# Kernel tuning notes

Measured on AMD Instinct MI355X. Metric: run time of the kernel, lower is better.

The kernel has to match this reference:

```python
import jax, jax.numpy as jnp
import numpy as np

N_NODES = 100000
IN_F = 512
HID = 256
HEADS = 1
CLASSES = 40
ALPHA = 0.5
EPS = 1e-5


def layer_norm(x, g, b):
    mu = jnp.mean(x, axis=-1, keepdims=True)
    var = jnp.mean(jnp.square(x - mu), axis=-1, keepdims=True)
    return g * (x - mu) / jnp.sqrt(var + EPS) + b


def full_attention_conv(qs, ks, vs):
    # qs, ks, vs: [N, H, D]; global (Frobenius) L2 normalization as in torch.norm(p=2)
    qs = qs / jnp.linalg.norm(qs.reshape(-1))
    ks = ks / jnp.linalg.norm(ks.reshape(-1))
    N = qs.shape[0]
    kvs = jnp.einsum('lhm,lhd->hmd', ks, vs)                  # [H, D, D]
    attention_num = jnp.einsum('nhm,hmd->nhd', qs, kvs) + N * vs
    ks_sum = jnp.sum(ks, axis=0)                              # [H, D]
    attention_normalizer = jnp.einsum('nhm,hm->nh', qs, ks_sum)[..., None] + N
    return attention_num / attention_normalizer               # [N, H, D]


def trans_layer(h, prev, Wq, bq, Wk, bk, Wv, bv, ln_g, ln_b):
    N = h.shape[0]
    q = (h @ Wq + bq).reshape(N, HEADS, HID)
    k = (h @ Wk + bk).reshape(N, HEADS, HID)
    v = (h @ Wv + bv).reshape(N, HEADS, HID)
    attn = full_attention_conv(q, k, v).mean(axis=1)          # [N, HID]
    h = ALPHA * attn + (1.0 - ALPHA) * prev
    return layer_norm(h, ln_g, ln_b)


def setup_inputs() -> dict:
    key = jax.random.key(0)
    ks = jax.random.split(key, 16)
    s_in = 1.0 / np.sqrt(IN_F)
    s_h = 1.0 / np.sqrt(HID)
    d = {
        'x': jax.random.normal(ks[0], (N_NODES, IN_F), jnp.float32),
        'edge_index': jax.random.randint(ks[1], (2, 1600000), 0, N_NODES, jnp.int64),
        'W_in': jax.random.normal(ks[2], (IN_F, HID), jnp.float32) * s_in,
        'b_in': jnp.zeros((HID,), jnp.float32),
        'ln0_g': jnp.ones((HID,), jnp.float32),
        'ln0_b': jnp.zeros((HID,), jnp.float32),
        'Wq0': jax.random.normal(ks[3], (HID, HID * HEADS), jnp.float32) * s_h,
        'bq0': jnp.zeros((HID * HEADS,), jnp.float32),
        'Wk0': jax.random.normal(ks[4], (HID, HID * HEADS), jnp.float32) * s_h,
        'bk0': jnp.zeros((HID * HEADS,), jnp.float32),
        'Wv0': jax.random.normal(ks[5], (HID, HID * HEADS), jnp.float32) * s_h,
        'bv0': jnp.zeros((HID * HEADS,), jnp.float32),
        'ln1_g': jnp.ones((HID,), jnp.float32),
        'ln1_b': jnp.zeros((HID,), jnp.float32),
        'Wq1': jax.random.normal(ks[6], (HID, HID * HEADS), jnp.float32) * s_h,
        'bq1': jnp.zeros((HID * HEADS,), jnp.float32),
        'Wk1': jax.random.normal(ks[7], (HID, HID * HEADS), jnp.float32) * s_h,
        'bk1': jnp.zeros((HID * HEADS,), jnp.float32),
        'Wv1': jax.random.normal(ks[8], (HID, HID * HEADS), jnp.float32) * s_h,
        'bv1': jnp.zeros((HID * HEADS,), jnp.float32),
        'ln2_g': jnp.ones((HID,), jnp.float32),
        'ln2_b': jnp.zeros((HID,), jnp.float32),
        'W_out': jax.random.normal(ks[9], (HID, CLASSES), jnp.float32) * s_h,
        'b_out': jnp.zeros((CLASSES,), jnp.float32),
    }
    return d


def reference(x, edge_index, W_in, b_in, ln0_g, ln0_b,
              Wq0, bq0, Wk0, bk0, Wv0, bv0, ln1_g, ln1_b,
              Wq1, bq1, Wk1, bk1, Wv1, bv1, ln2_g, ln2_b,
              W_out, b_out):
    # SGFormer forward with use_graph=False, eval mode (dropout no-op).
    h = jax.nn.relu(layer_norm(x @ W_in + b_in, ln0_g, ln0_b))
    prev = h
    h = trans_layer(h, prev, Wq0, bq0, Wk0, bk0, Wv0, bv0, ln1_g, ln1_b)
    prev = h
    h = trans_layer(h, prev, Wq1, bq1, Wk1, bk1, Wv1, bv1, ln2_g, ln2_b)
    return h @ W_out + b_out  # [N, CLASSES]
```

## Files before the change

kernel.cpp:

```cpp
#include <hip/hip_runtime.h>


typedef __attribute__((ext_vector_type(8))) short short8;
typedef __attribute__((ext_vector_type(4))) short short4v;
typedef __attribute__((ext_vector_type(4))) float floatx4;

__device__ __forceinline__ float bf2f(short u) {
    union { unsigned int i; float f; } v;
    v.i = ((unsigned int)(unsigned short)u) << 16;
    return v.f;
}
__device__ __forceinline__ short f2bf(float f) {
    union { float f; unsigned int i; } v; v.f = f;
    unsigned int b = v.i + 0x7fffu + ((v.i >> 16) & 1u);
    return (short)(b >> 16);
}

#define HID 256
#define MROWS 100000
#define GBLK 1563
#define EPSLN 1e-5f

__device__ __forceinline__ size_t fragoff(int blk, int w, int m, int n, int lane) {
    return (((((size_t)blk * 4 + w) * 4 + m) * 4 + n) * 64 + lane);
}

__device__ __forceinline__ void stage_a256(const short* __restrict__ A, short* As,
                                           int row0, int wave, int lane)
{
    const int base = wave * 512;
#pragma unroll
    for (int it = 0; it < 8; ++it) {
        int J = base + it * 64 + lane;
        int row = J >> 5, jj = J & 31;
        int c = jj ^ (row & 31);
        int rowg = min(row0 + row, MROWS - 1);
        const short* gp = A + (size_t)rowg * HID + c * 8;
        __builtin_amdgcn_global_load_lds(
            (const __attribute__((address_space(1))) void*)gp,
            (__attribute__((address_space(3))) void*)&As[(size_t)(base + it * 64) * 8],
            16, 0, 0);
    }
}
__device__ __forceinline__ void stage_lin256(const short* __restrict__ A, short* As,
                                             int row0, int wave, int lane)
{
    const int base = wave * 512;
#pragma unroll
    for (int it = 0; it < 8; ++it) {
        int J = base + it * 64 + lane;
        int row = J >> 5, jj = J & 31;
        int rowg = min(row0 + row, MROWS - 1);
        const short* gp = A + (size_t)rowg * HID + jj * 8;
        __builtin_amdgcn_global_load_lds(
            (const __attribute__((address_space(1))) void*)gp,
            (__attribute__((address_space(3))) void*)&As[(size_t)(base + it * 64) * 8],
            16, 0, 0);
    }
}
__device__ __forceinline__ short8 read_a256(const short* As, int m, int ki, int quad, int l15)
{
    int row = m * 16 + l15;
    int phys = (ki * 4 + quad) ^ (row & 31);
    return *(const short8*)&As[((size_t)row * 32 + phys) * 8];
}

__global__ __launch_bounds__(256, 3)
void qkv_kernel(const short* __restrict__ h,
                const short* __restrict__ BTq, const short* __restrict__ BTk,
                const short* __restrict__ BTv,
                const float* __restrict__ bq, const float* __restrict__ bk,
                const float* __restrict__ bv,
                short* __restrict__ qO, short* __restrict__ kF, short* __restrict__ vF,
                float* __restrict__ sqq, float* __restrict__ sqk,
                float* __restrict__ ksum)
{
    __shared__ short As[64 * 256];
    __shared__ short Cb[16 * 264];

    const int tid = threadIdx.x, wave = tid >> 6, lane = tid & 63;
    const int quad = lane >> 4, l15 = lane & 15;
    const int blk = blockIdx.x;
    const int row0 = blk * 64, nb = wave * 64;

    stage_a256(h, As, row0, wave, lane);
    __syncthreads();

    floatx4 acc[4][4];

    auto gemm256 = [&](const short* __restrict__ BT) {
#pragma unroll
        for (int m = 0; m < 4; m++)
#pragma unroll
            for (int n = 0; n < 4; n++) acc[m][n] = (floatx4)0.0f;
#pragma unroll
        for (int ki = 0; ki < 8; ++ki) {
            short8 a[4];
#pragma unroll
            for (int m = 0; m < 4; ++m) a[m] = read_a256(As, m, ki, quad, l15);
#pragma unroll
            for (int n = 0; n < 4; ++n) {
                short8 b = *(const short8*)(BT + (size_t)(nb + n * 16 + l15) * 256 + ki * 32 + quad * 8);
#pragma unroll
                for (int m = 0; m < 4; ++m)
                    acc[m][n] = __builtin_amdgcn_mfma_f32_16x16x32_bf16(a[m], b, acc[m][n], 0, 0, 0);
            }
        }
    };

    float bn[4];

    gemm256(BTk);
#pragma unroll
    for (int n = 0; n < 4; n++) bn[n] = bk[nb + n * 16 + l15];
    {
        float ssq = 0.f;
        float csum[4] = {0.f, 0.f, 0.f, 0.f};
#pragma unroll
        for (int m = 0; m < 4; m++)
#pragma unroll
            for (int r = 0; r < 4; r++) {
                int rl = m * 16 + quad * 4 + r;
                bool valid = (row0 + rl) < MROWS;
#pragma unroll
                for (int n = 0; n < 4; n++) {
                    float val = acc[m][n][r] + bn[n];
                    acc[m][n][r] = val;
                    if (valid) { ssq += val * val; csum[n] += val; }
                }
            }
#pragma unroll
        for (int off = 32; off; off >>= 1) ssq += __shfl_down(ssq, off);
        if (lane == 0) atomicAdd(sqk, ssq);
#pragma unroll
        for (int n = 0; n < 4; n++) {
            float cv = csum[n];
            cv += __shfl_xor(cv, 16);
            cv += __shfl_xor(cv, 32);
            if (quad == 0) atomicAdd(&ksum[nb + n * 16 + l15], cv);
        }
#pragma unroll
        for (int m = 0; m < 4; ++m)
#pragma unroll
            for (int n = 0; n < 4; ++n) {
                short4v s4;
#pragma unroll
                for (int r = 0; r < 4; ++r) s4[r] = f2bf(acc[m][n][r]);
                *(short4v*)(kF + fragoff(blk, wave, m, n, lane) * 4) = s4;
            }
    }

    gemm256(BTv);
#pragma unroll
    for (int n = 0; n < 4; n++) bn[n] = bv[nb + n * 16 + l15];
#pragma unroll
    for (int m = 0; m < 4; ++m)
#pragma unroll
        for (int n = 0; n < 4; ++n) {
            short4v s4;
#pragma unroll
            for (int r = 0; r < 4; ++r) s4[r] = f2bf(acc[m][n][r] + bn[n]);
            *(short4v*)(vF + fragoff(blk, wave, m, n, lane) * 4) = s4;
        }

    gemm256(BTq);
#pragma unroll
    for (int n = 0; n < 4; n++) bn[n] = bq[nb + n * 16 + l15];
    {
        float ssq = 0.f;
#pragma unroll
        for (int m = 0; m < 4; m++)
#pragma unroll
            for (int r = 0; r < 4; r++) {
                int rl = m * 16 + quad * 4 + r;
                bool valid = (row0 + rl) < MROWS;
#pragma unroll
                for (int n = 0; n < 4; n++) {
                    float val = acc[m][n][r] + bn[n];
                    acc[m][n][r] = val;
                    if (valid) ssq += val * val;
                }
            }
#pragma unroll
        for (int off = 32; off; off >>= 1) ssq += __shfl_down(ssq, off);
        if (lane == 0) atomicAdd(sqq, ssq);
    }
#pragma unroll
    for (int m = 0; m < 4; ++m) {
        __syncthreads();
#pragma unroll
        for (int n = 0; n < 4; ++n)
#pragma unroll
            for (int r = 0; r < 4; ++r)
                Cb[(quad * 4 + r) * 264 + nb + n * 16 + l15] = f2bf(acc[m][n][r]);
        __syncthreads();
#pragma unroll
        for (int ch = tid; ch < 512; ch += 256) {
            int rl = ch >> 5, co = (ch & 31) * 8;
            int row = row0 + m * 16 + rl;
            if (row < MROWS)
                *(short8*)(qO + (size_t)row * 256 + co) = *(const short8*)&Cb[rl * 264 + co];
        }
    }
}

__global__ __launch_bounds__(256, 3)
void attn_kernel(const short* __restrict__ q, const short* __restrict__ KVt,
                 const short* __restrict__ vF, short* __restrict__ h,
                 const float* __restrict__ lng, const float* __restrict__ lnb,
                 float Nf)
{
    __shared__ short As[64 * 256];
    __shared__ float denA[64];
    __shared__ float redS[64][4], redQ[64][4];
    short* Cb = As;
    float* rowm = (float*)&As[4352];
    float* rowr = (float*)&As[4480];

    const int tid = threadIdx.x, wave = tid >> 6, lane = tid & 63;
    const int quad = lane >> 4, l15 = lane & 15;
    const int blk = blockIdx.x;
    const int row0 = blk * 64, nb = wave * 64;

    stage_a256(q, As, row0, wave, lane);
    __syncthreads();

    floatx4 acc[4][4];
#pragma unroll
    for (int m = 0; m < 4; m++)
#pragma unroll
        for (int n = 0; n < 4; n++) acc[m][n] = (floatx4)0.0f;
    floatx4 accd[4];
#pragma unroll
    for (int m = 0; m < 4; m++) accd[m] = (floatx4)0.0f;

#pragma unroll
    for (int ki = 0; ki < 8; ++ki) {
        short8 a[4];
#pragma unroll
        for (int m = 0; m < 4; ++m) a[m] = read_a256(As, m, ki, quad, l15);
#pragma unroll
        for (int n = 0; n < 4; ++n) {
            short8 b = *(const short8*)(KVt + (size_t)(nb + n * 16 + l15) * 256 + ki * 32 + quad * 8);
#pragma unroll
            for (int m = 0; m < 4; ++m)
                acc[m][n] = __builtin_amdgcn_mfma_f32_16x16x32_bf16(a[m], b, acc[m][n], 0, 0, 0);
        }
        if (wave == 0) {
            short8 bd = *(const short8*)(KVt + (size_t)(256 + l15) * 256 + ki * 32 + quad * 8);
#pragma unroll
            for (int m = 0; m < 4; ++m)
                accd[m] = __builtin_amdgcn_mfma_f32_16x16x32_bf16(a[m], bd, accd[m], 0, 0, 0);
        }
    }
    short4v vr[4][4];
#pragma unroll
    for (int m = 0; m < 4; ++m)
#pragma unroll
        for (int n = 0; n < 4; ++n)
            vr[m][n] = *(const short4v*)(vF + fragoff(blk, wave, m, n, lane) * 4);

    if (wave == 0 && l15 == 0) {
#pragma unroll
        for (int m = 0; m < 4; m++)
#pragma unroll
            for (int r = 0; r < 4; r++)
                denA[m * 16 + quad * 4 + r] = accd[m][r];
    }
    __syncthreads();

    stage_lin256(h, As, row0, wave, lane);

#pragma unroll
    for (int m = 0; m < 4; m++)
#pragma unroll
        for (int r = 0; r < 4; r++) {
            int rl = m * 16 + quad * 4 + r;
            float rden = 1.0f / (denA[rl] + Nf);
#pragma unroll
            for (int n = 0; n < 4; n++)
                acc[m][n][r] = 0.5f * (acc[m][n][r] + Nf * bf2f(vr[m][n][r])) * rden;
        }
    __syncthreads();

#pragma unroll
    for (int m = 0; m < 4; m++)
#pragma unroll
        for (int r = 0; r < 4; r++) {
            int rl = m * 16 + quad * 4 + r;
            float s = 0.f, s2 = 0.f;
#pragma unroll
            for (int n = 0; n < 4; n++) {
                int col = nb + n * 16 + l15;
                float pv = bf2f(As[(size_t)rl * 256 + col]);
                float val = acc[m][n][r] + 0.5f * pv;
                acc[m][n][r] = val;
                s += val; s2 += val * val;
            }
#pragma unroll
            for (int off = 1; off < 16; off <<= 1) {
                s += __shfl_xor(s, off);
                s2 += __shfl_xor(s2, off);
            }
            if (l15 == 0) { redS[rl][wave] = s; redQ[rl][wave] = s2; }
        }
    __syncthreads();
    if (tid < 64) {
        float s = redS[tid][0] + redS[tid][1] + redS[tid][2] + redS[tid][3];
        float s2 = redQ[tid][0] + redQ[tid][1] + redQ[tid][2] + redQ[tid][3];
        float mean = s * (1.0f / 256.0f);
        float var = s2 * (1.0f / 256.0f) - mean * mean;
        rowm[tid] = mean;
        rowr[tid] = rsqrtf(var + EPSLN);
    }
    float g[4], bb[4];
#pragma unroll
    for (int n = 0; n < 4; n++) {
        g[n] = lng[nb + n * 16 + l15];
        bb[n] = lnb[nb + n * 16 + l15];
    }
#pragma unroll
    for (int m = 0; m < 4; ++m) {
        __syncthreads();
#pragma unroll
        for (int n = 0; n < 4; ++n)
#pragma unroll
            for (int r = 0; r < 4; ++r) {
                int rl = m * 16 + quad * 4 + r;
                float x = (acc[m][n][r] - rowm[rl]) * rowr[rl] * g[n] + bb[n];
                Cb[(quad * 4 + r) * 264 + nb + n * 16 + l15] = f2bf(x);
            }
        __syncthreads();
#pragma unroll
        for (int ch = tid; ch < 512; ch += 256) {
            int rl = ch >> 5, co = (ch & 31) * 8;
            int row = row0 + m * 16 + rl;
            if (row < MROWS)
                *(short8*)(h + (size_t)row * 256 + co) = *(const short8*)&Cb[rl * 264 + co];
        }
    }
}

__global__ __launch_bounds__(256, 3)
void in_kernel(const float* __restrict__ x, const short* __restrict__ WinT,
               const float* __restrict__ b_in, const float* __restrict__ lng,
               const float* __restrict__ lnb, short* __restrict__ h)
{
    __shared__ short As[2][64 * 128];
    __shared__ short Cb[16 * 264];
    __shared__ float redS[64][4], redQ[64][4];
    __shared__ float rowm[64], rowr[64];

    const int tid = threadIdx.x, wave = tid >> 6, lane = tid & 63;
    const int quad = lane >> 4, l15 = lane & 15;
    const int row0 = blockIdx.x * 64, nb = wave * 64;

    floatx4 acc[4][4];
#pragma unroll
    for (int m = 0; m < 4; m++)
#pragma unroll
        for (int n = 0; n < 4; n++) acc[m][n] = (floatx4)0.0f;

    floatx4 xr[4][2];
    auto issue = [&](int slab) {
#pragma unroll
        for (int it = 0; it < 4; ++it) {
            int J = it * 256 + tid;
            int row = J >> 4, jj = J & 15, c = jj ^ (row & 15);
            int rowg = min(row0 + row, MROWS - 1);
            const float* gp = x + (size_t)rowg * 512 + slab + c * 8;
            xr[it][0] = *(const floatx4*)gp;
            xr[it][1] = *(const floatx4*)(gp + 4);
        }
    };
    auto commit = [&](short* dst) {
#pragma unroll
        for (int it = 0; it < 4; ++it) {
            int J = it * 256 + tid;
            short8 s8;
#pragma unroll
            for (int i = 0; i < 4; ++i) { s8[i] = f2bf(xr[it][0][i]); s8[i + 4] = f2bf(xr[it][1][i]); }
            *(short8*)&dst[(size_t)J * 8] = s8;
        }
    };

    issue(0);
    commit(As[0]);
    __syncthreads();

#pragma unroll
    for (int s = 0; s < 4; ++s) {
        if (s < 3) issue((s + 1) * 128);
        const short* cur = As[s & 1];
#pragma unroll
        for (int ki = 0; ki < 4; ++ki) {
            short8 a[4];
#pragma unroll
            for (int m = 0; m < 4; ++m) {
                int row = m * 16 + l15;
                int phys = (ki * 4 + quad) ^ (row & 15);
                a[m] = *(const short8*)&cur[((size_t)row * 16 + phys) * 8];
            }
#pragma unroll
            for (int n = 0; n < 4; ++n) {
                short8 b = *(const short8*)(WinT + (size_t)(nb + n * 16 + l15) * 512 + s * 128 + ki * 32 + quad * 8);
#pragma unroll
                for (int m = 0; m < 4; ++m)
                    acc[m][n] = __builtin_amdgcn_mfma_f32_16x16x32_bf16(a[m], b, acc[m][n], 0, 0, 0);
            }
        }
        if (s < 3) {
            commit(As[(s + 1) & 1]);
            __syncthreads();
        }
    }
    float bn[4];
#pragma unroll
    for (int n = 0; n < 4; n++) bn[n] = b_in[nb + n * 16 + l15];
#pragma unroll
    for (int m = 0; m < 4; m++)
#pragma unroll
        for (int r = 0; r < 4; r++) {
            int rl = m * 16 + quad * 4 + r;
            float s = 0.f, s2 = 0.f;
#pragma unroll
            for (int n = 0; n < 4; n++) {
                float val = acc[m][n][r] + bn[n];
                acc[m][n][r] = val;
                s += val; s2 += val * val;
            }
#pragma unroll
            for (int off = 1; off < 16; off <<= 1) {
                s += __shfl_xor(s, off);
                s2 += __shfl_xor(s2, off);
            }
            if (l15 == 0) { redS[rl][wave] = s; redQ[rl][wave] = s2; }
        }
    __syncthreads();
    if (tid < 64) {
        float s = redS[tid][0] + redS[tid][1] + redS[tid][2] + redS[tid][3];
        float s2 = redQ[tid][0] + redQ[tid][1] + redQ[tid][2] + redQ[tid][3];
        float mean = s * (1.0f / 256.0f);
        float var = s2 * (1.0f / 256.0f) - mean * mean;
        rowm[tid] = mean;
        rowr[tid] = rsqrtf(var + EPSLN);
    }
    __syncthreads();
    float g[4], bb[4];
#pragma unroll
    for (int n = 0; n < 4; n++) {
        g[n] = lng[nb + n * 16 + l15];
        bb[n] = lnb[nb + n * 16 + l15];
    }
#pragma unroll
    for (int m = 0; m < 4; ++m) {
        __syncthreads();
#pragma unroll
        for (int n = 0; n < 4; ++n)
#pragma unroll
            for (int r = 0; r < 4; ++r) {
                int rl = m * 16 + quad * 4 + r;
                float xv = (acc[m][n][r] - rowm[rl]) * rowr[rl] * g[n] + bb[n];
                Cb[(quad * 4 + r) * 264 + nb + n * 16 + l15] = f2bf(fmaxf(xv, 0.f));
            }
        __syncthreads();
#pragma unroll
        for (int ch = tid; ch < 512; ch += 256) {
            int rl = ch >> 5, co = (ch & 31) * 8;
            int row = row0 + m * 16 + rl;
            if (row < MROWS)
                *(short8*)(h + (size_t)row * 256 + co) = *(const short8*)&Cb[rl * 264 + co];
        }
    }
}

__global__ __launch_bounds__(256)
void kv_kernel(const short* __restrict__ kF, const short* __restrict__ vF,
               float* __restrict__ KV, int M)
{
    __shared__ short ksT[128][40];
    __shared__ short vsT[128][40];
    const int t = threadIdx.x, wave = t >> 6, lane = t & 63;
    const int quad = lane >> 4, l15 = lane & 15;
    const int mb = blockIdx.x * 128, nbb = blockIdx.y * 128;
    const int bbeg = blockIdx.z * 7;
    const int bend = min(GBLK, bbeg + 7);

    floatx4 acc[2][8];
#pragma unroll
    for (int m = 0; m < 2; m++)
#pragma unroll
        for (int j = 0; j < 8; j++) acc[m][j] = (floatx4)0.0f;

    const int wm = wave * 32;

    short4v kc[4], vc[4];
    auto loadstripe = [&](int blk, int half) {
#pragma unroll
        for (int i = 0; i < 4; ++i) {
            int ci = t + i * 256;
            int colc = ci & 127, rowg = ci >> 7;
            int qs = rowg & 3, mi = rowg >> 2;
            int m = half * 2 + mi;
            bool valid = (blk * 64 + m * 16 + qs * 4) < M;
            int Ck = mb + colc, Cv = nbb + colc;
            size_t ok = fragoff(blk, Ck >> 6, m, (Ck >> 4) & 3, qs * 16 + (Ck & 15)) * 4;
            size_t ov = fragoff(blk, Cv >> 6, m, (Cv >> 4) & 3, qs * 16 + (Cv & 15)) * 4;
            kc[i] = valid ? *(const short4v*)(kF + ok) : (short4v)(short)0;
            vc[i] = valid ? *(const short4v*)(vF + ov) : (short4v)(short)0;
        }
    };
    auto commit = [&]() {
#pragma unroll
        for (int i = 0; i < 4; ++i) {
            int ci = t + i * 256;
            int colc = ci & 127, rowg = ci >> 7;
            *(short4v*)&ksT[colc][rowg * 4] = kc[i];
            *(short4v*)&vsT[colc][rowg * 4] = vc[i];
        }
    };

    loadstripe(bbeg, 0);
    for (int blk = bbeg; blk < bend; ++blk)
#pragma unroll
        for (int half = 0; half < 2; ++half) {
            __syncthreads();
            commit();
            __syncthreads();
            bool more = !(blk == bend - 1 && half == 1);
            short8 a0 = *(const short8*)&ksT[wm + l15][quad * 8];
            short8 a1 = *(const short8*)&ksT[wm + 16 + l15][quad * 8];
            if (more) loadstripe(half ? blk + 1 : blk, half ^ 1);
#pragma unroll
            for (int j = 0; j < 8; j++) {
                short8 b = *(const short8*)&vsT[j * 16 + l15][quad * 8];
                acc[0][j] = __builtin_amdgcn_mfma_f32_16x16x32_bf16(a0, b, acc[0][j], 0, 0, 0);
                acc[1][j] = __builtin_amdgcn_mfma_f32_16x16x32_bf16(a1, b, acc[1][j], 0, 0, 0);
            }
        }
#pragma unroll
    for (int mi = 0; mi < 2; mi++)
#pragma unroll
        for (int j = 0; j < 8; j++)
#pragma unroll
            for (int r = 0; r < 4; r++) {
                int m = mb + wm + mi * 16 + quad * 4 + r;
                int n = nbb + j * 16 + l15;
                atomicAdd(&KV[(size_t)m * HID + n], acc[mi][j][r]);
            }
}

__global__ void scale_kernel(const float* __restrict__ KV, const float* __restrict__ ksum,
                             const float* __restrict__ sq, short* __restrict__ KVt)
{
    float s = rsqrtf(sq[0]) * rsqrtf(sq[1]);
    int d = blockIdx.x;
    int m = threadIdx.x;
    float val;
    if (d < 256)       val = KV[(size_t)m * HID + d] * s;
    else if (d == 256) val = ksum[m] * s;
    else               val = 0.f;
    KVt[(size_t)d * HID + m] = f2bf(val);
}

__global__ __launch_bounds__(256)
void gemm_out(const short* __restrict__ A, const short* __restrict__ BT,
              const float* __restrict__ bias, float* __restrict__ Out, int M)
{
    const int tid = threadIdx.x, wave = tid >> 6, lane = tid & 63;
    const int quad = lane >> 4, l15 = lane & 15;
    const int row0 = blockIdx.x * 128 + wave * 32;
    const int K = 256;
    floatx4 acc[2][3];
#pragma unroll
    for (int m = 0; m < 2; m++)
#pragma unroll
        for (int n = 0; n < 3; n++) acc[m][n] = (floatx4)0.0f;

    int ra0 = min(row0 + l15, M - 1);
    int ra1 = min(row0 + 16 + l15, M - 1);
    for (int kk = 0; kk < K; kk += 32) {
        short8 a0 = *(const short8*)(A + (size_t)ra0 * K + kk + quad * 8);
        short8 a1 = *(const short8*)(A + (size_t)ra1 * K + kk + quad * 8);
#pragma unroll
        for (int n = 0; n < 3; n++) {
            int col = n * 16 + l15;
            short8 b = (short8)(short)0;
            if (col < 40) b = *(const short8*)(BT + (size_t)col * K + kk + quad * 8);
            acc[0][n] = __builtin_amdgcn_mfma_f32_16x16x32_bf16(a0, b, acc[0][n], 0, 0, 0);
            acc[1][n] = __builtin_amdgcn_mfma_f32_16x16x32_bf16(a1, b, acc[1][n], 0, 0, 0);
        }
    }
#pragma unroll
    for (int m = 0; m < 2; m++)
#pragma unroll
        for (int n = 0; n < 3; n++)
#pragma unroll
            for (int r = 0; r < 4; r++) {
                int row = row0 + m * 16 + quad * 4 + r;
                int col = n * 16 + l15;
                if (row < M && col < 40)
                    Out[(size_t)row * 40 + col] = acc[m][n][r] + bias[col];
            }
}

struct TJobs { const float* src[8]; short* dst[8]; int R[8]; int C[8]; };

__global__ void wtrans(TJobs j)
{
    int job = blockIdx.y;
    int R = j.R[job], Cc = j.C[job];
    const float* s = j.src[job];
    short* d = j.dst[job];
    int n = R * Cc;
    for (int idx = blockIdx.x * 256 + threadIdx.x; idx < n; idx += gridDim.x * 256) {
        int r = idx / Cc, c = idx - r * Cc;
        d[(size_t)c * R + r] = f2bf(s[idx]);
    }
}

__global__ void zerof(float* p, int n)
{
    int i = blockIdx.x * 256 + threadIdx.x;
    if (i < n) p[i] = 0.f;
}

extern "C" void kernel_launch(void* const* d_in, const int* in_sizes, int n_in,
                              void* d_out, int out_size, void* d_ws, size_t ws_size,
                              hipStream_t stream)
{
    const float* x    = (const float*)d_in[0];
    const float* W_in = (const float*)d_in[2];
    const float* b_in = (const float*)d_in[3];
    const float* ln0g = (const float*)d_in[4];
    const float* ln0b = (const float*)d_in[5];
    const float* Wq0  = (const float*)d_in[6];  const float* bq0 = (const float*)d_in[7];
    const float* Wk0  = (const float*)d_in[8];  const float* bk0 = (const float*)d_in[9];
    const float* Wv0  = (const float*)d_in[10]; const float* bv0 = (const float*)d_in[11];
    const float* ln1g = (const float*)d_in[12]; const float* ln1b = (const float*)d_in[13];
    const float* Wq1  = (const float*)d_in[14]; const float* bq1 = (const float*)d_in[15];
    const float* Wk1  = (const float*)d_in[16]; const float* bk1 = (const float*)d_in[17];
    const float* Wv1  = (const float*)d_in[18]; const float* bv1 = (const float*)d_in[19];
    const float* ln2g = (const float*)d_in[20]; const float* ln2b = (const float*)d_in[21];
    const float* W_out = (const float*)d_in[22]; const float* b_out = (const float*)d_in[23];

    const int M = MROWS;
    const int MPAD = GBLK * 64;
    char* ws = (char*)d_ws;
    size_t off = 0;
    auto alloc = [&](size_t bytes) -> char* {
        char* p = ws + off;
        off += (bytes + 255) & ~(size_t)255;
        return p;
    };
    short* h = (short*)alloc((size_t)M * HID * 2);
    short* q = (short*)alloc((size_t)M * HID * 2);
    short* k = (short*)alloc((size_t)MPAD * HID * 2);
    short* v = (short*)alloc((size_t)MPAD * HID * 2);
    short* WinT  = (short*)alloc((size_t)512 * 256 * 2);
    short* WqT0  = (short*)alloc((size_t)65536 * 2);
    short* WkT0  = (short*)alloc((size_t)65536 * 2);
    short* WvT0  = (short*)alloc((size_t)65536 * 2);
    short* WqT1  = (short*)alloc((size_t)65536 * 2);
    short* WkT1  = (short*)alloc((size_t)65536 * 2);
    short* WvT1  = (short*)alloc((size_t)65536 * 2);
    short* WoutT = (short*)alloc((size_t)40 * 256 * 2);
    float* zbase = (float*)alloc((size_t)(65536 * 2 + 256 * 2 + 4) * 4);
    float* KV0 = zbase;
    float* KV1 = zbase + 65536;
    float* ksum0 = zbase + 131072;
    float* ksum1 = ksum0 + 256;
    float* sq = ksum1 + 256;
    short* KVt0 = (short*)alloc((size_t)272 * 256 * 2);
    short* KVt1 = (short*)alloc((size_t)272 * 256 * 2);

    const int ZN = 65536 * 2 + 256 * 2 + 4;
    zerof<<<dim3((ZN + 255) / 256), 256, 0, stream>>>(zbase, ZN);

    TJobs tj;
    tj.src[0] = W_in;  tj.dst[0] = WinT;  tj.R[0] = 512; tj.C[0] = 256;
    tj.src[1] = Wq0;   tj.dst[1] = WqT0;  tj.R[1] = 256; tj.C[1] = 256;
    tj.src[2] = Wk0;   tj.dst[2] = WkT0;  tj.R[2] = 256; tj.C[2] = 256;
    tj.src[3] = Wv0;   tj.dst[3] = WvT0;  tj.R[3] = 256; tj.C[3] = 256;
    tj.src[4] = Wq1;   tj.dst[4] = WqT1;  tj.R[4] = 256; tj.C[4] = 256;
    tj.src[5] = Wk1;   tj.dst[5] = WkT1;  tj.R[5] = 256; tj.C[5] = 256;
    tj.src[6] = Wv1;   tj.dst[6] = WvT1;  tj.R[6] = 256; tj.C[6] = 256;
    tj.src[7] = W_out; tj.dst[7] = WoutT; tj.R[7] = 256; tj.C[7] = 40;
    wtrans<<<dim3(512, 8), 256, 0, stream>>>(tj);

    const int GB = GBLK;
    const float Nf = (float)M;
    const int ZB = (GBLK + 6) / 7;

    in_kernel<<<GB, 256, 0, stream>>>(x, WinT, b_in, ln0g, ln0b, h);
    qkv_kernel<<<GB, 256, 0, stream>>>(h, WqT0, WkT0, WvT0, bq0, bk0, bv0,
                                       q, k, v, sq + 0, sq + 1, ksum0);
    kv_kernel<<<dim3(2, 2, ZB), 256, 0, stream>>>(k, v, KV0, M);
    scale_kernel<<<272, 256, 0, stream>>>(KV0, ksum0, sq + 0, KVt0);
    attn_kernel<<<GB, 256, 0, stream>>>(q, KVt0, v, h, ln1g, ln1b, Nf);
    qkv_kernel<<<GB, 256, 0, stream>>>(h, WqT1, WkT1, WvT1, bq1, bk1, bv1,
                                       q, k, v, sq + 2, sq + 3, ksum1);
    kv_kernel<<<dim3(2, 2, ZB), 256, 0, stream>>>(k, v, KV1, M);
    scale_kernel<<<272, 256, 0, stream>>>(KV1, ksum1, sq + 2, KVt1);
    attn_kernel<<<GB, 256, 0, stream>>>(q, KVt1, v, h, ln2g, ln2b, Nf);
    gemm_out<<<(M + 127) / 128, 256, 0, stream>>>(h, WoutT, b_out, (float*)d_out, M);
}
```

Before: 1.143 ms.

## Pack K/V fragments into 16-byte stores and hierarchically reduce sum-of-squares atomics

Changes the fragment layout for the K and V intermediates so each lane writes and reads 8 bf16 values (two adjacent n-tiles) per access instead of 4, widening global stores and loads in the QKV and attention kernels. Sum-of-squares reductions now go through a shared-memory accumulator per block, so only one global atomic per block is issued instead of one per wave. The Q GEMM is moved first in the QKV kernel. The reduction adds extra block barriers, and the KV reduction kernel's index math now has to decode the new packed layout.

```diff
diff --git a/kernel.cpp b/kernel.cpp
--- a/kernel.cpp
+++ b/kernel.cpp
@@ -21,8 +21,8 @@
 #define GBLK 1563
 #define EPSLN 1e-5f
 
-__device__ __forceinline__ size_t fragoff(int blk, int w, int m, int n, int lane) {
-    return (((((size_t)blk * 4 + w) * 4 + m) * 4 + n) * 64 + lane);
+__device__ __forceinline__ size_t frag16off(int blk, int w, int m, int p, int lane) {
+    return (((((size_t)blk * 4 + w) * 4 + m) * 2 + p) * 64 + lane);
 }
 
 __device__ __forceinline__ void stage_a256(const short* __restrict__ A, short* As,
@@ -77,6 +77,7 @@
 {
     __shared__ short As[64 * 256];
     __shared__ short Cb[16 * 264];
+    __shared__ float scr;
 
     const int tid = threadIdx.x, wave = tid >> 6, lane = tid & 63;
     const int quad = lane >> 4, l15 = lane & 15;
@@ -109,6 +110,50 @@
     };
 
     float bn[4];
+
+    gemm256(BTq);
+#pragma unroll
+    for (int n = 0; n < 4; n++) bn[n] = bq[nb + n * 16 + l15];
+    {
+        float ssq = 0.f;
+#pragma unroll
+        for (int m = 0; m < 4; m++)
+#pragma unroll
+            for (int r = 0; r < 4; r++) {
+                int rl = m * 16 + quad * 4 + r;
+                bool valid = (row0 + rl) < MROWS;
+#pragma unroll
+                for (int n = 0; n < 4; n++) {
+                    float val = acc[m][n][r] + bn[n];
+                    acc[m][n][r] = val;
+                    if (valid) ssq += val * val;
+                }
+            }
+#pragma unroll
+        for (int off = 32; off; off >>= 1) ssq += __shfl_down(ssq, off);
+        if (tid == 0) scr = 0.f;
+        __syncthreads();
+        if (lane == 0) atomicAdd(&scr, ssq);
+        __syncthreads();
+        if (tid == 0) atomicAdd(sqq, scr);
+    }
+#pragma unroll
+    for (int m = 0; m < 4; ++m) {
+        __syncthreads();
+#pragma unroll
+        for (int n = 0; n < 4; ++n)
+#pragma unroll
+            for (int r = 0; r < 4; ++r)
+                Cb[(quad * 4 + r) * 264 + nb + n * 16 + l15] = f2bf(acc[m][n][r]);
+        __syncthreads();
+#pragma unroll
+        for (int ch = tid; ch < 512; ch += 256) {
+            int rl = ch >> 5, co = (ch & 31) * 8;
+            int row = row0 + m * 16 + rl;
+            if (row < MROWS)
+                *(short8*)(qO + (size_t)row * 256 + co) = *(const short8*)&Cb[rl * 264 + co];
+        }
+    }
 
     gemm256(BTk);
 #pragma unroll
@@ -131,7 +176,11 @@
             }
 #pragma unroll
         for (int off = 32; off; off >>= 1) ssq += __shfl_down(ssq, off);
-        if (lane == 0) atomicAdd(sqk, ssq);
+        if (tid == 0) scr = 0.f;
+        __syncthreads();
+        if (lane == 0) atomicAdd(&scr, ssq);
+        __syncthreads();
+        if (tid == 0) atomicAdd(sqk, scr);
 #pragma unroll
         for (int n = 0; n < 4; n++) {
             float cv = csum[n];
@@ -142,11 +191,14 @@
 #pragma unroll
         for (int m = 0; m < 4; ++m)
 #pragma unroll
-            for (int n = 0; n < 4; ++n) {
-                short4v s4;
-#pragma unroll
-                for (int r = 0; r < 4; ++r) s4[r] = f2bf(acc[m][n][r]);
-                *(short4v*)(kF + fragoff(blk, wave, m, n, lane) * 4) = s4;
+            for (int p = 0; p < 2; ++p) {
+                short8 s8;
+#pragma unroll
+                for (int r = 0; r < 4; ++r) {
+                    s8[r]     = f2bf(acc[m][2 * p][r]);
+                    s8[4 + r] = f2bf(acc[m][2 * p + 1][r]);
+                }
+                *(short8*)(kF + frag16off(blk, wave, m, p, lane) * 8) = s8;
             }
     }
 
@@ -156,52 +208,15 @@
 #pragma unroll
     for (int m = 0; m < 4; ++m)
 #pragma unroll
-        for (int n = 0; n < 4; ++n) {
-            short4v s4;
-#pragma unroll
-            for (int r = 0; r < 4; ++r) s4[r] = f2bf(acc[m][n][r] + bn[n]);
-            *(short4v*)(vF + fragoff(blk, wave, m, n, lane) * 4) = s4;
-        }
-
-    gemm256(BTq);
-#pragma unroll
-    for (int n = 0; n < 4; n++) bn[n] = bq[nb + n * 16 + l15];
-    {
-        float ssq = 0.f;
-#pragma unroll
-        for (int m = 0; m < 4; m++)
-#pragma unroll
-            for (int r = 0; r < 4; r++) {
-                int rl = m * 16 + quad * 4 + r;
-                bool valid = (row0 + rl) < MROWS;
-#pragma unroll
-                for (int n = 0; n < 4; n++) {
-                    float val = acc[m][n][r] + bn[n];
-                    acc[m][n][r] = val;
-                    if (valid) ssq += val * val;
-                }
-            }
-#pragma unroll
-        for (int off = 32; off; off >>= 1) ssq += __shfl_down(ssq, off);
-        if (lane == 0) atomicAdd(sqq, ssq);
-    }
-#pragma unroll
-    for (int m = 0; m < 4; ++m) {
-        __syncthreads();
-#pragma unroll
-        for (int n = 0; n < 4; ++n)
-#pragma unroll
-            for (int r = 0; r < 4; ++r)
-                Cb[(quad * 4 + r) * 264 + nb + n * 16 + l15] = f2bf(acc[m][n][r]);
-        __syncthreads();
-#pragma unroll
-        for (int ch = tid; ch < 512; ch += 256) {
-            int rl = ch >> 5, co = (ch & 31) * 8;
-            int row = row0 + m * 16 + rl;
-            if (row < MROWS)
-                *(short8*)(qO + (size_t)row * 256 + co) = *(const short8*)&Cb[rl * 264 + co];
-        }
-    }
+        for (int p = 0; p < 2; ++p) {
+            short8 s8;
+#pragma unroll
+            for (int r = 0; r < 4; ++r) {
+                s8[r]     = f2bf(acc[m][2 * p][r] + bn[2 * p]);
+                s8[4 + r] = f2bf(acc[m][2 * p + 1][r] + bn[2 * p + 1]);
+            }
+            *(short8*)(vF + frag16off(blk, wave, m, p, lane) * 8) = s8;
+        }
 }
 
 __global__ __launch_bounds__(256, 3)
@@ -253,12 +268,12 @@
                 accd[m] = __builtin_amdgcn_mfma_f32_16x16x32_bf16(a[m], bd, accd[m], 0, 0, 0);
         }
     }
-    short4v vr[4][4];
+    short8 vp[4][2];
 #pragma unroll
     for (int m = 0; m < 4; ++m)
 #pragma unroll
-        for (int n = 0; n < 4; ++n)
-            vr[m][n] = *(const short4v*)(vF + fragoff(blk, wave, m, n, lane) * 4);
+        for (int p = 0; p < 2; ++p)
+            vp[m][p] = *(const short8*)(vF + frag16off(blk, wave, m, p, lane) * 8);
 
     if (wave == 0 && l15 == 0) {
 #pragma unroll
@@ -278,8 +293,10 @@
             int rl = m * 16 + quad * 4 + r;
             float rden = 1.0f / (denA[rl] + Nf);
 #pragma unroll
-            for (int n = 0; n < 4; n++)
-                acc[m][n][r] = 0.5f * (acc[m][n][r] + Nf * bf2f(vr[m][n][r])) * rden;
+            for (int n = 0; n < 4; n++) {
+                float vv = bf2f(vp[m][n >> 1][(n & 1) * 4 + r]);
+                acc[m][n][r] = 0.5f * (acc[m][n][r] + Nf * vv) * rden;
+            }
         }
     __syncthreads();
 
@@ -504,8 +521,10 @@
             int m = half * 2 + mi;
             bool valid = (blk * 64 + m * 16 + qs * 4) < M;
             int Ck = mb + colc, Cv = nbb + colc;
-            size_t ok = fragoff(blk, Ck >> 6, m, (Ck >> 4) & 3, qs * 16 + (Ck & 15)) * 4;
-            size_t ov = fragoff(blk, Cv >> 6, m, (Cv >> 4) & 3, qs * 16 + (Cv & 15)) * 4;
+            size_t ok = frag16off(blk, Ck >> 6, m, (Ck >> 5) & 1, qs * 16 + (Ck & 15)) * 8
+                        + (size_t)((Ck >> 4) & 1) * 4;
+            size_t ov = frag16off(blk, Cv >> 6, m, (Cv >> 5) & 1, qs * 16 + (Cv & 15)) * 8
+                        + (size_t)((Cv >> 4) & 1) * 4;
             kc[i] = valid ? *(const short4v*)(kF + ok) : (short4v)(short)0;
             vc[i] = valid ? *(const short4v*)(vF + ov) : (short4v)(short)0;
         }
```

Measured after the change: 997.9 us. 1.15x faster.
